# Kernel tuning notes

Measured on AMD Instinct MI355X. Metric: run time of the kernel, lower is better.

The kernel has to match this reference:

```python
import jax, jax.numpy as jnp
import numpy as np

_SAMPLING_EPS = 1e-05
_RMAX = 0.9999999403953552          # largest float32 uniform from tl.rand
_RMAX_LOG = -5.960464477539063e-08  # log(_RMAX)


def setup_inputs() -> dict:
    key = jax.random.key(0)
    k1, k2, k3, k4, k5 = jax.random.split(key, 5)
    B, V = 256, 128000
    logits = jax.random.normal(k1, (B, V), dtype=jnp.float32) * 4.0
    temperature = jax.random.uniform(k2, (B,), dtype=jnp.float32, minval=0.1, maxval=1.5)
    top_k = jax.random.randint(k3, (B,), 1, 1000).astype(jnp.int32)
    top_p = jax.random.uniform(k4, (B,), dtype=jnp.float32, minval=0.5, maxval=1.0)
    gumbel_u = jax.random.uniform(k5, (B, V), dtype=jnp.float32)
    return {
        "logits": logits,
        "temperature": temperature,
        "top_k": top_k,
        "top_p": top_p,
        "gumbel_u": gumbel_u,
        "num_logprobs": 20,
    }


def reference(logits, temperature, top_k, top_p, gumbel_u, num_logprobs):
    B, V = logits.shape
    # --- apply_temperature: divide by temp, temp<eps treated as 1.0 (greedy) ---
    temp = jnp.where(temperature < _SAMPLING_EPS, 1.0, temperature)
    logits = logits.astype(jnp.float32) / temp[:, None]

    # --- apply_top_k_top_p: sort ascending, mask, scatter back ---
    idx_sort = jnp.argsort(logits, axis=-1)                      # ascending
    logits_sort = jnp.take_along_axis(logits, idx_sort, axis=-1)
    # top-k: value of the k-th largest is at position V-k in ascending order
    k_pos = (V - top_k.astype(jnp.int32))[:, None]
    thresh = jnp.take_along_axis(logits_sort, k_pos, axis=-1)    # [B,1]
    logits_sort = jnp.where(logits_sort < thresh, -jnp.inf, logits_sort)
    # top-p: drop ascending prefix whose cumulative prob <= 1-p (keep last)
    probs_sort = jax.nn.softmax(logits_sort, axis=-1)
    cum = jnp.cumsum(probs_sort, axis=-1)
    mask_p = cum <= (1.0 - top_p)[:, None]
    mask_p = mask_p.at[:, -1].set(False)
    logits_sort = jnp.where(mask_p, -jnp.inf, logits_sort)
    # unsort back to vocab order
    inv = jnp.argsort(idx_sort, axis=-1)
    logits_f = jnp.take_along_axis(logits_sort, inv, axis=-1)

    # --- softmax + gumbel-trick sampling: argmax(p / -log(u)) ---
    probs = jax.nn.softmax(logits_f, axis=-1)
    q = -jnp.where(gumbel_u >= _RMAX, _RMAX_LOG, jnp.log(gumbel_u))
    greedy = (temperature < _SAMPLING_EPS)[:, None]  # kernel skips these rows
    ratio = jnp.where(greedy, probs, probs / q)
    sampled = jnp.argmax(ratio, axis=-1)             # [B]

    # --- gather_logprobs ---
    logprobs = jax.nn.log_softmax(logits_f, axis=-1)
    sampled_lp = jnp.take_along_axis(logprobs, sampled[:, None], axis=-1)  # [B,1]
    ranks = jnp.sum(logprobs > sampled_lp, axis=-1)                        # [B]
    topk_lp, topk_idx = jax.lax.top_k(logprobs, num_logprobs)
    indices = jnp.concatenate([sampled[:, None], topk_idx], axis=1)        # [B,1+K]
    lp_vals = jnp.concatenate([sampled_lp, topk_lp], axis=1)               # [B,1+K]

    return sampled[:, None], indices, lp_vals, ranks
```

## Files before the change

kernel.cpp:

```cpp
#include <hip/hip_runtime.h>
#include <math.h>

#define NTHR 1024
#define CAP 4096
#define BINS 4096

#define RMAX_F 0.9999999403953552f
#define RMAX_LOG_F -5.960464477539063e-08f
#define NEG_BIG -3.0e38f

__device__ __forceinline__ unsigned keyOf(float v) {
    unsigned b = __float_as_uint(v);
    return (b & 0x80000000u) ? ~b : (b | 0x80000000u);
}
__device__ __forceinline__ float valOfKey(unsigned k) {
    unsigned b = (k & 0x80000000u) ? (k ^ 0x80000000u) : ~k;
    return __uint_as_float(b);
}

__global__ __launch_bounds__(NTHR) void sampler_kernel(
    const float* __restrict__ logits,
    const float* __restrict__ temperature,
    const int* __restrict__ top_kv,
    const float* __restrict__ top_pv,
    const float* __restrict__ gumbel,
    float* __restrict__ out,
    int B, int V, int K)
{
    const int r = blockIdx.x;
    const int tid = threadIdx.x;
    const int lane = tid & 63;

    __shared__ unsigned long long cand[CAP];
    __shared__ int scanI[NTHR];
    __shared__ float varr[1024];
    __shared__ float Earr[1024];
    __shared__ float sfx[1024];
    __shared__ unsigned char flagArr[1024];
    __shared__ unsigned bitmap[64];
    __shared__ unsigned s_prefix;
    __shared__ int s_cntgt, s_total, s_lvl;
    __shared__ int s_ncand, s_nkeep, s_rank, s_g0, s_g1;
    __shared__ unsigned long long s_amax;
    __shared__ float s_vs;

    unsigned* hist = (unsigned*)cand;

    const float* row = logits + (long long)r * V;
    const float* urow = gumbel + (long long)r * V;

    float traw = temperature[r];
    bool greedy = traw < 1e-5f;
    float t = greedy ? 1.0f : traw;
    int k = top_kv[r];
    if (k < 1) k = 1;
    if (k > V) k = V;
    float p = top_pv[r];

    const float4* row4 = (const float4*)row;
    const int V4 = V >> 2;
    const int Vt = V4 << 2;
    const unsigned cpy = tid & 1u;

    for (int i = tid; i < BINS * 2; i += NTHR) hist[i] = 0;
    __syncthreads();
    for (int i = tid; i < V4; i += NTHR) {
        float4 l4 = row4[i];
        unsigned k0 = keyOf(l4.x), k1 = keyOf(l4.y), k2 = keyOf(l4.z), k3 = keyOf(l4.w);
        atomicAdd(&hist[((k0 >> 20) << 1) | cpy], 1u);
        atomicAdd(&hist[((k1 >> 20) << 1) | cpy], 1u);
        atomicAdd(&hist[((k2 >> 20) << 1) | cpy], 1u);
        atomicAdd(&hist[((k3 >> 20) << 1) | cpy], 1u);
    }
    for (int i = Vt + tid; i < V; i += NTHR) {
        unsigned key = keyOf(row[i]);
        atomicAdd(&hist[((key >> 20) << 1) | cpy], 1u);
    }
    __syncthreads();
    {
        int base = tid << 2;
        int cs = 0;
        #pragma unroll
        for (int j = 0; j < 4; ++j)
            cs += (int)(hist[(base + j) * 2] + hist[(base + j) * 2 + 1]);
        scanI[tid] = cs;
    }
    __syncthreads();
    for (int d = 1; d < NTHR; d <<= 1) {
        int v = (tid + d < NTHR) ? scanI[tid + d] : 0;
        __syncthreads();
        scanI[tid] += v;
        __syncthreads();
    }
    {
        int mine = scanI[tid];
        int above = (tid + 1 < NTHR) ? scanI[tid + 1] : 0;
        if (mine >= k && above < k) {
            int base = tid << 2;
            int run = above;
            for (int b = base + 3; b >= base; --b) {
                int mb = (int)(hist[b * 2] + hist[b * 2 + 1]);
                if (run + mb >= k) {
                    s_prefix = (unsigned)b; s_cntgt = run; s_total = run + mb; s_lvl = 0;
                    break;
                }
                run += mb;
            }
        }
    }
    for (int level = 1; level <= 2; ++level) {
        __syncthreads();
        if (s_total <= CAP) break;
        for (int i = tid; i < 512; i += NTHR) hist[i] = 0;
        __syncthreads();
        unsigned pfx = s_prefix;
        const int msh = 32 - (12 + 8 * (level - 1));
        const int bsh = msh - 8;
        for (int i = tid; i < V4; i += NTHR) {
            float4 l4 = row4[i];
            float vv[4] = { l4.x, l4.y, l4.z, l4.w };
            #pragma unroll
            for (int j = 0; j < 4; ++j) {
                unsigned key = keyOf(vv[j]);
                if ((key >> msh) == pfx)
                    atomicAdd(&hist[(((key >> bsh) & 255u) << 1) | cpy], 1u);
            }
        }
        for (int i = Vt + tid; i < V; i += NTHR) {
            unsigned key = keyOf(row[i]);
            if ((key >> msh) == pfx)
                atomicAdd(&hist[(((key >> bsh) & 255u) << 1) | cpy], 1u);
        }
        __syncthreads();
        if (tid == 0) {
            int run = s_cntgt;
            for (int b = 255; b >= 0; --b) {
                int mb = (int)(hist[b * 2] + hist[b * 2 + 1]);
                if (run + mb >= k) {
                    s_prefix = (pfx << 8) | (unsigned)b; s_cntgt = run; s_total = run + mb;
                    break;
                }
                run += mb;
            }
            s_lvl = level;
        }
    }
    __syncthreads();
    const unsigned tlo = s_prefix << (20 - 8 * s_lvl);
    if (tid == 0) s_ncand = 0;
    __syncthreads();

    for (int i = tid; i < V4; i += NTHR) {
        float4 l4 = row4[i];
        float vv[4] = { l4.x, l4.y, l4.z, l4.w };
        #pragma unroll
        for (int j = 0; j < 4; ++j) {
            unsigned key = keyOf(vv[j]);
            bool pred = (key >= tlo);
            unsigned long long mask = __ballot(pred ? 1 : 0);
            if (mask) {
                int leader = __ffsll(mask) - 1;
                int cnt = __popcll(mask);
                int base = 0;
                if (lane == leader) base = atomicAdd(&s_ncand, cnt);
                base = __shfl(base, leader);
                if (pred) {
                    int pos = base + __popcll(mask & ((1ULL << lane) - 1ULL));
                    if (pos < CAP) {
                        unsigned gidx = (unsigned)(i * 4 + j);
                        cand[pos] = ((unsigned long long)key << 32) | (unsigned)(~gidx);
                    }
                }
            }
        }
    }
    for (int i = Vt + tid; i < V; i += NTHR) {
        unsigned key = keyOf(row[i]);
        bool pred = (key >= tlo);
        unsigned long long mask = __ballot(pred ? 1 : 0);
        if (mask) {
            int leader = __ffsll(mask) - 1;
            int cnt = __popcll(mask);
            int base = 0;
            if (lane == leader) base = atomicAdd(&s_ncand, cnt);
            base = __shfl(base, leader);
            if (pred) {
                int pos = base + __popcll(mask & ((1ULL << lane) - 1ULL));
                if (pos < CAP) {
                    unsigned gidx = (unsigned)i;
                    cand[pos] = ((unsigned long long)key << 32) | (unsigned)(~gidx);
                }
            }
        }
    }
    __syncthreads();
    int ncand = s_ncand; if (ncand > CAP) ncand = CAP;
    if (k > ncand) k = ncand;

    int P = 2; while (P < ncand) P <<= 1;
    for (int i = ncand + tid; i < P; i += NTHR) cand[i] = 0ULL;
    __syncthreads();
    for (int size = 2; size <= P; size <<= 1) {
        for (int stride = size >> 1; stride > 0; stride >>= 1) {
            for (int i = tid; i < P; i += NTHR) {
                int j = i ^ stride;
                if (j > i) {
                    unsigned long long a = cand[i], b = cand[j];
                    bool up = ((i & size) == 0);
                    bool sw = up ? (a < b) : (a > b);
                    if (sw) { cand[i] = b; cand[j] = a; }
                }
            }
            __syncthreads();
        }
    }

    for (int i = tid; i < 1024; i += NTHR)
        varr[i] = (i < ncand) ? (valOfKey((unsigned)(cand[i] >> 32)) / t) : NEG_BIG;
    __syncthreads();

    const float m = varr[0];
    const float tkeyV = varr[k - 1];
    int ntop = k;
    while (ntop < ncand) {
        float vi = (ntop < 1024) ? varr[ntop]
                                 : (valOfKey((unsigned)(cand[ntop] >> 32)) / t);
        if (vi != tkeyV) break;
        ++ntop;
    }
    if (ntop > 1024) ntop = 1024;

    for (int i = tid; i < 1024; i += NTHR) {
        float e = (i < ntop) ? expf(varr[i] - m) : 0.0f;
        Earr[i] = e;
        sfx[i] = e;
    }
    __syncthreads();
    for (int d = 1; d < 1024; d <<= 1) {
        float t0 = (tid + d < 1024) ? sfx[tid + d] : 0.0f;
        __syncthreads();
        sfx[tid] += t0;
        __syncthreads();
    }
    const float Zp = sfx[0];
    const float cmp = 1.0f - p;
    if (tid == 0) { s_nkeep = 0; s_rank = 0; s_amax = 0ULL; }
    for (int i = tid; i < 64; i += NTHR) bitmap[i] = 0;
    __syncthreads();
    {
        int local = 0;
        for (int i = tid; i < ntop; i += NTHR)
            if (sfx[i] / Zp > cmp) local++;
        if (local) atomicAdd(&s_nkeep, local);
    }
    __syncthreads();
    const int nkeep = s_nkeep;
    if (tid == 0) {
        float vb = varr[nkeep - 1];
        int g0 = nkeep - 1;
        while (g0 > 0 && varr[g0 - 1] == vb) --g0;
        int g1 = nkeep;
        while (g1 < ntop && varr[g1] == vb) ++g1;
        s_g0 = g0; s_g1 = g1;
    }
    __syncthreads();
    const int g0 = s_g0, g1 = s_g1;
    const int mkeep = nkeep - g0;
    for (int i = g0 + tid; i < g1; i += NTHR) {
        unsigned gi = ~(unsigned)(cand[i] & 0xFFFFFFFFull);
        int rk = 0;
        for (int j = g0; j < g1; ++j) {
            unsigned gj = ~(unsigned)(cand[j] & 0xFFFFFFFFull);
            if (gj > gi) rk++;
        }
        flagArr[i] = (rk < mkeep) ? 1 : 0;
    }
    __syncthreads();

    const float Z2 = (nkeep < 1024) ? (Zp - sfx[nkeep]) : Zp;
    const float L = logf(Z2);

    for (int i = tid; i < g1; i += NTHR) {
        if (i < g0 || flagArr[i]) {
            unsigned lo = (unsigned)(cand[i] & 0xFFFFFFFFull);
            unsigned gidx = ~lo;
            float u = urow[gidx];
            float q = -((u >= RMAX_F) ? RMAX_LOG_F : logf(u));
            float prob = Earr[i] / Z2;
            float ratio = greedy ? prob : (prob / q);
            unsigned long long comp = ((unsigned long long)__float_as_uint(ratio) << 32) | lo;
            atomicMax(&s_amax, comp);
            if (gidx < 2048) atomicOr(&bitmap[gidx >> 5], 1u << (gidx & 31));
        }
    }
    __syncthreads();
    const unsigned samp_lo = (unsigned)(s_amax & 0xFFFFFFFFull);
    const unsigned samp = ~samp_lo;
    for (int i = tid; i < ntop; i += NTHR)
        if ((unsigned)(cand[i] & 0xFFFFFFFFull) == samp_lo) s_vs = varr[i];
    __syncthreads();
    const float lp_s = (s_vs - m) - L;
    {
        int local = 0;
        for (int i = tid; i < nkeep; i += NTHR)
            if ((varr[i] - m) - L > lp_s) local++;
        if (local) atomicAdd(&s_rank, local);
    }
    __syncthreads();

    if (tid == 0) {
        float* o_samp = out;
        float* o_idx  = out + B;
        float* o_lp   = out + B + (long long)B * (K + 1);
        float* o_rank = out + B + 2LL * B * (K + 1);
        long long rowo = (long long)r * (K + 1);

        o_samp[r] = (float)samp;
        o_idx[rowo] = (float)samp;
        o_lp[rowo] = lp_s;
        o_rank[r] = (float)s_rank;

        int ntk = (nkeep < K) ? nkeep : K;
        int slot = 0, i = 0;
        while (slot < ntk && i < g1) {
            float v = varr[i];
            int re = i + 1;
            while (re < g1 && varr[re] == v) ++re;
            long long last = -1;
            while (slot < ntk) {
                unsigned best = 0xFFFFFFFFu;
                for (int j = i; j < re; ++j) {
                    if (j >= g0 && !flagArr[j]) continue;
                    unsigned gj = ~(unsigned)(cand[j] & 0xFFFFFFFFull);
                    if ((long long)gj > last && gj < best) best = gj;
                }
                if (best == 0xFFFFFFFFu) break;
                o_idx[rowo + 1 + slot] = (float)best;
                o_lp[rowo + 1 + slot] = (v - m) - L;
                last = best; ++slot;
            }
            i = re;
        }
        if (nkeep < K) {
            int j = 0;
            for (int c = nkeep; c < K; ++c) {
                while (bitmap[j >> 5] & (1u << (j & 31))) ++j;
                o_idx[rowo + 1 + c] = (float)j;
                o_lp[rowo + 1 + c] = NEG_BIG;
                ++j;
            }
        }
    }
}

extern "C" void kernel_launch(void* const* d_in, const int* in_sizes, int n_in,
                              void* d_out, int out_size, void* d_ws, size_t ws_size,
                              hipStream_t stream) {
    const float* logits      = (const float*)d_in[0];
    const float* temperature = (const float*)d_in[1];
    const int*   top_k       = (const int*)d_in[2];
    const float* top_p       = (const float*)d_in[3];
    const float* gumbel      = (const float*)d_in[4];
    int B = in_sizes[1];
    int V = in_sizes[0] / B;
    int K = (out_size / B - 4) / 2;
    sampler_kernel<<<B, NTHR, 0, stream>>>(logits, temperature, top_k, top_p,
                                           gumbel, (float*)d_out, B, V, K);
}
```

Measured before the change: 317.9 us.

## Estimate top-k threshold from sampled histogram with exact fallback

The top-k threshold search now builds its coarse histogram from a 1/8 subsample of the row. It picks a conservative threshold bin from the scaled k plus slack, then compacts the candidates in one full pass. If the candidate count falls below k or above capacity, it falls back to the original exact multi-level radix search. The compaction loop is also unrolled to issue four float4 loads at once. The aim is to replace a full histogram pass, and sometimes the refinement passes, with a cheap sampled pass, at the cost of possible extra work on fallback rows.

```diff
diff --git a/kernel.cpp b/kernel.cpp
--- a/kernel.cpp
+++ b/kernel.cpp
@@ -38,6 +38,8 @@
     __shared__ float sfx[1024];
     __shared__ unsigned char flagArr[1024];
     __shared__ unsigned bitmap[64];
+    __shared__ unsigned s_tlo;
+    __shared__ int s_fallback;
     __shared__ unsigned s_prefix;
     __shared__ int s_cntgt, s_total, s_lvl;
     __shared__ int s_ncand, s_nkeep, s_rank, s_g0, s_g1;
@@ -62,101 +64,12 @@
     const int Vt = V4 << 2;
     const unsigned cpy = tid & 1u;
 
-    for (int i = tid; i < BINS * 2; i += NTHR) hist[i] = 0;
-    __syncthreads();
-    for (int i = tid; i < V4; i += NTHR) {
-        float4 l4 = row4[i];
-        unsigned k0 = keyOf(l4.x), k1 = keyOf(l4.y), k2 = keyOf(l4.z), k3 = keyOf(l4.w);
-        atomicAdd(&hist[((k0 >> 20) << 1) | cpy], 1u);
-        atomicAdd(&hist[((k1 >> 20) << 1) | cpy], 1u);
-        atomicAdd(&hist[((k2 >> 20) << 1) | cpy], 1u);
-        atomicAdd(&hist[((k3 >> 20) << 1) | cpy], 1u);
-    }
-    for (int i = Vt + tid; i < V; i += NTHR) {
-        unsigned key = keyOf(row[i]);
-        atomicAdd(&hist[((key >> 20) << 1) | cpy], 1u);
-    }
-    __syncthreads();
-    {
-        int base = tid << 2;
-        int cs = 0;
-        #pragma unroll
-        for (int j = 0; j < 4; ++j)
-            cs += (int)(hist[(base + j) * 2] + hist[(base + j) * 2 + 1]);
-        scanI[tid] = cs;
-    }
-    __syncthreads();
-    for (int d = 1; d < NTHR; d <<= 1) {
-        int v = (tid + d < NTHR) ? scanI[tid + d] : 0;
-        __syncthreads();
-        scanI[tid] += v;
-        __syncthreads();
-    }
-    {
-        int mine = scanI[tid];
-        int above = (tid + 1 < NTHR) ? scanI[tid + 1] : 0;
-        if (mine >= k && above < k) {
-            int base = tid << 2;
-            int run = above;
-            for (int b = base + 3; b >= base; --b) {
-                int mb = (int)(hist[b * 2] + hist[b * 2 + 1]);
-                if (run + mb >= k) {
-                    s_prefix = (unsigned)b; s_cntgt = run; s_total = run + mb; s_lvl = 0;
-                    break;
-                }
-                run += mb;
-            }
-        }
-    }
-    for (int level = 1; level <= 2; ++level) {
-        __syncthreads();
-        if (s_total <= CAP) break;
-        for (int i = tid; i < 512; i += NTHR) hist[i] = 0;
-        __syncthreads();
-        unsigned pfx = s_prefix;
-        const int msh = 32 - (12 + 8 * (level - 1));
-        const int bsh = msh - 8;
-        for (int i = tid; i < V4; i += NTHR) {
-            float4 l4 = row4[i];
-            float vv[4] = { l4.x, l4.y, l4.z, l4.w };
-            #pragma unroll
-            for (int j = 0; j < 4; ++j) {
-                unsigned key = keyOf(vv[j]);
-                if ((key >> msh) == pfx)
-                    atomicAdd(&hist[(((key >> bsh) & 255u) << 1) | cpy], 1u);
-            }
-        }
-        for (int i = Vt + tid; i < V; i += NTHR) {
-            unsigned key = keyOf(row[i]);
-            if ((key >> msh) == pfx)
-                atomicAdd(&hist[(((key >> bsh) & 255u) << 1) | cpy], 1u);
-        }
-        __syncthreads();
-        if (tid == 0) {
-            int run = s_cntgt;
-            for (int b = 255; b >= 0; --b) {
-                int mb = (int)(hist[b * 2] + hist[b * 2 + 1]);
-                if (run + mb >= k) {
-                    s_prefix = (pfx << 8) | (unsigned)b; s_cntgt = run; s_total = run + mb;
-                    break;
-                }
-                run += mb;
-            }
-            s_lvl = level;
-        }
-    }
-    __syncthreads();
-    const unsigned tlo = s_prefix << (20 - 8 * s_lvl);
-    if (tid == 0) s_ncand = 0;
-    __syncthreads();
-
-    for (int i = tid; i < V4; i += NTHR) {
-        float4 l4 = row4[i];
+    auto procF4 = [&](float4 l4, int i4) {
         float vv[4] = { l4.x, l4.y, l4.z, l4.w };
         #pragma unroll
         for (int j = 0; j < 4; ++j) {
             unsigned key = keyOf(vv[j]);
-            bool pred = (key >= tlo);
+            bool pred = (key >= s_tlo);
             unsigned long long mask = __ballot(pred ? 1 : 0);
             if (mask) {
                 int leader = __ffsll(mask) - 1;
@@ -167,33 +80,184 @@
                 if (pred) {
                     int pos = base + __popcll(mask & ((1ULL << lane) - 1ULL));
                     if (pos < CAP) {
-                        unsigned gidx = (unsigned)(i * 4 + j);
+                        unsigned gidx = (unsigned)(i4 * 4 + j);
                         cand[pos] = ((unsigned long long)key << 32) | (unsigned)(~gidx);
                     }
                 }
             }
         }
-    }
-    for (int i = Vt + tid; i < V; i += NTHR) {
-        unsigned key = keyOf(row[i]);
-        bool pred = (key >= tlo);
-        unsigned long long mask = __ballot(pred ? 1 : 0);
-        if (mask) {
-            int leader = __ffsll(mask) - 1;
-            int cnt = __popcll(mask);
-            int base = 0;
-            if (lane == leader) base = atomicAdd(&s_ncand, cnt);
-            base = __shfl(base, leader);
-            if (pred) {
-                int pos = base + __popcll(mask & ((1ULL << lane) - 1ULL));
-                if (pos < CAP) {
-                    unsigned gidx = (unsigned)i;
-                    cand[pos] = ((unsigned long long)key << 32) | (unsigned)(~gidx);
-                }
-            }
-        }
-    }
-    __syncthreads();
+    };
+    auto compact = [&]() {
+        int i = tid;
+        for (; i + 3 * NTHR < V4; i += 4 * NTHR) {
+            float4 a0 = row4[i];
+            float4 a1 = row4[i + NTHR];
+            float4 a2 = row4[i + 2 * NTHR];
+            float4 a3 = row4[i + 3 * NTHR];
+            procF4(a0, i); procF4(a1, i + NTHR);
+            procF4(a2, i + 2 * NTHR); procF4(a3, i + 3 * NTHR);
+        }
+        for (; i < V4; i += NTHR) { float4 a = row4[i]; procF4(a, i); }
+        for (int j = Vt + tid; j < V; j += NTHR) {
+            unsigned key = keyOf(row[j]);
+            bool pred = (key >= s_tlo);
+            unsigned long long mask = __ballot(pred ? 1 : 0);
+            if (mask) {
+                int leader = __ffsll(mask) - 1;
+                int cnt = __popcll(mask);
+                int base = 0;
+                if (lane == leader) base = atomicAdd(&s_ncand, cnt);
+                base = __shfl(base, leader);
+                if (pred) {
+                    int pos = base + __popcll(mask & ((1ULL << lane) - 1ULL));
+                    if (pos < CAP)
+                        cand[pos] = ((unsigned long long)key << 32) | (unsigned)(~(unsigned)j);
+                }
+            }
+        }
+    };
+
+    for (int i = tid; i < BINS * 2; i += NTHR) hist[i] = 0;
+    __syncthreads();
+    for (int i = tid; i < V4; i += NTHR * 8) {
+        float4 l4 = row4[i];
+        atomicAdd(&hist[((keyOf(l4.x) >> 20) << 1) | cpy], 1u);
+        atomicAdd(&hist[((keyOf(l4.y) >> 20) << 1) | cpy], 1u);
+        atomicAdd(&hist[((keyOf(l4.z) >> 20) << 1) | cpy], 1u);
+        atomicAdd(&hist[((keyOf(l4.w) >> 20) << 1) | cpy], 1u);
+    }
+    __syncthreads();
+    {
+        int base = tid << 2;
+        int cs = 0;
+        #pragma unroll
+        for (int j = 0; j < 4; ++j)
+            cs += (int)(hist[(base + j) * 2] + hist[(base + j) * 2 + 1]);
+        scanI[tid] = cs;
+    }
+    __syncthreads();
+    for (int d = 1; d < NTHR; d <<= 1) {
+        int v = (tid + d < NTHR) ? scanI[tid + d] : 0;
+        __syncthreads();
+        scanI[tid] += v;
+        __syncthreads();
+    }
+    const int S = scanI[0];
+    long long ks = ((long long)k * S) / V;
+    const int starg = (int)ks + 40 + (int)(ks >> 2);
+    if (tid == 0) s_fallback = (2 * starg > S) ? 1 : 0;
+    __syncthreads();
+    if (!s_fallback) {
+        int mine = scanI[tid];
+        int above = (tid + 1 < NTHR) ? scanI[tid + 1] : 0;
+        if (mine >= starg && above < starg) {
+            int base = tid << 2;
+            int run = above;
+            for (int b = base + 3; b >= base; --b) {
+                int mb = (int)(hist[b * 2] + hist[b * 2 + 1]);
+                if (run + mb >= starg) { s_tlo = (unsigned)b << 20; break; }
+                run += mb;
+            }
+        }
+        __syncthreads();
+        if (tid == 0) s_ncand = 0;
+        __syncthreads();
+        compact();
+        __syncthreads();
+        if (tid == 0) s_fallback = (s_ncand < k || s_ncand > CAP) ? 1 : 0;
+    }
+    __syncthreads();
+
+    if (s_fallback) {
+        for (int i = tid; i < BINS * 2; i += NTHR) hist[i] = 0;
+        __syncthreads();
+        for (int i = tid; i < V4; i += NTHR) {
+            float4 l4 = row4[i];
+            atomicAdd(&hist[((keyOf(l4.x) >> 20) << 1) | cpy], 1u);
+            atomicAdd(&hist[((keyOf(l4.y) >> 20) << 1) | cpy], 1u);
+            atomicAdd(&hist[((keyOf(l4.z) >> 20) << 1) | cpy], 1u);
+            atomicAdd(&hist[((keyOf(l4.w) >> 20) << 1) | cpy], 1u);
+        }
+        for (int i = Vt + tid; i < V; i += NTHR)
+            atomicAdd(&hist[((keyOf(row[i]) >> 20) << 1) | cpy], 1u);
+        __syncthreads();
+        {
+            int base = tid << 2;
+            int cs = 0;
+            #pragma unroll
+            for (int j = 0; j < 4; ++j)
+                cs += (int)(hist[(base + j) * 2] + hist[(base + j) * 2 + 1]);
+            scanI[tid] = cs;
+        }
+        __syncthreads();
+        for (int d = 1; d < NTHR; d <<= 1) {
+            int v = (tid + d < NTHR) ? scanI[tid + d] : 0;
+            __syncthreads();
+            scanI[tid] += v;
+            __syncthreads();
+        }
+        {
+            int mine = scanI[tid];
+            int above = (tid + 1 < NTHR) ? scanI[tid + 1] : 0;
+            if (mine >= k && above < k) {
+                int base = tid << 2;
+                int run = above;
+                for (int b = base + 3; b >= base; --b) {
+                    int mb = (int)(hist[b * 2] + hist[b * 2 + 1]);
+                    if (run + mb >= k) {
+                        s_prefix = (unsigned)b; s_cntgt = run;
+                        s_total = run + mb; s_lvl = 0;
+                        break;
+                    }
+                    run += mb;
+                }
+            }
+        }
+        for (int level = 1; level <= 2; ++level) {
+            __syncthreads();
+            if (s_total <= CAP) break;
+            for (int i = tid; i < 512; i += NTHR) hist[i] = 0;
+            __syncthreads();
+            unsigned pfx = s_prefix;
+            const int msh = 32 - (12 + 8 * (level - 1));
+            const int bsh = msh - 8;
+            for (int i = tid; i < V4; i += NTHR) {
+                float4 l4 = row4[i];
+                float vv[4] = { l4.x, l4.y, l4.z, l4.w };
+                #pragma unroll
+                for (int j = 0; j < 4; ++j) {
+                    unsigned key = keyOf(vv[j]);
+                    if ((key >> msh) == pfx)
+                        atomicAdd(&hist[(((key >> bsh) & 255u) << 1) | cpy], 1u);
+                }
+            }
+            for (int i = Vt + tid; i < V; i += NTHR) {
+                unsigned key = keyOf(row[i]);
+                if ((key >> msh) == pfx)
+                    atomicAdd(&hist[(((key >> bsh) & 255u) << 1) | cpy], 1u);
+            }
+            __syncthreads();
+            if (tid == 0) {
+                int run = s_cntgt;
+                for (int b = 255; b >= 0; --b) {
+                    int mb = (int)(hist[b * 2] + hist[b * 2 + 1]);
+                    if (run + mb >= k) {
+                        s_prefix = (pfx << 8) | (unsigned)b;
+                        s_cntgt = run; s_total = run + mb;
+                        break;
+                    }
+                    run += mb;
+                }
+                s_lvl = level;
+            }
+        }
+        __syncthreads();
+        if (tid == 0) { s_tlo = s_prefix << (20 - 8 * s_lvl); s_ncand = 0; }
+        __syncthreads();
+        compact();
+        __syncthreads();
+    }
+
     int ncand = s_ncand; if (ncand > CAP) ncand = CAP;
     if (k > ncand) k = ncand;
 
```

After: 323.2 us. No clear change (+1.7%).
